# Optimization experiments

Hardware: AMD Instinct MI355X
Metric: run time of the kernel (lower is better)

## Reference

```python
import jax, jax.numpy as jnp
import numpy as np

N_IN, N_OUT = 1024, 4096
D_IN = 1024          # next power of two of N_IN (no padding needed)
STACK = 4            # ceil(N_OUT / D_IN)
BATCH = 8192


def fwht0(x):
    """Unnormalized fast Walsh-Hadamard transform along axis 0 of a (D, C) matrix."""
    D, C = x.shape
    h = 1
    while h < D:
        y = x.reshape(D // (2 * h), 2, h, C)
        a, b = y[:, 0], y[:, 1]
        x = jnp.stack([a + b, a - b], axis=1).reshape(D, C)
        h *= 2
    return x


def sample_block(s1, s2, g_mu, g_rho, eps):
    # W = diag(s1) @ H @ diag(g_tilde) @ H @ diag(s2)
    g_tilde = g_mu + jax.nn.softplus(g_rho) * eps            # (D,)
    Hs2 = fwht0(jnp.diag(s2))                                # H @ diag(s2)
    W = s1[:, None] * fwht0(g_tilde[:, None] * Hs2)          # (D, D)
    return W


def setup_inputs() -> dict:
    key = jax.random.key(0)
    k = jax.random.split(key, 6)
    return {
        "x": jax.random.normal(k[0], (BATCH, N_IN), dtype=jnp.float32),
        "s1": jax.random.normal(k[1], (STACK, D_IN), dtype=jnp.float32),
        "s2": jax.random.normal(k[2], (STACK, D_IN), dtype=jnp.float32),
        "g_mu": jax.random.normal(k[3], (STACK, D_IN), dtype=jnp.float32),
        "g_rho": jax.random.uniform(k[4], (STACK, D_IN), dtype=jnp.float32) - 3.0,
        "eps": jax.random.normal(k[5], (STACK, D_IN), dtype=jnp.float32),
    }


def reference(x, s1, s2, g_mu, g_rho, eps):
    # Sample all stacked square blocks and concatenate rows -> (D_out, D_in)
    Ws = jax.vmap(sample_block)(s1, s2, g_mu, g_rho, eps)    # (stack, D, D)
    W = Ws.reshape(STACK * D_IN, D_IN)                       # (D_out, D_in)
    # Pad input to D_in (no-op here since N_IN == D_IN, kept for fidelity)
    x_padded = jnp.pad(x, ((0, 0), (0, D_IN - N_IN)))
    out = x_padded @ W.T                                     # (B, D_out)
    return out[..., :N_OUT]
```

## Files before the change

kernel.cpp:

```cpp
#include <hip/hip_runtime.h>
#include <math.h>

#define D_IN   1024
#define STACKN 4
#define BATCHN 8192
#define OUTW   (STACKN * D_IN)

__device__ __forceinline__ float softplus_f(float x) {
    return fmaxf(x, 0.0f) + log1pf(expf(-fabsf(x)));
}

__device__ __forceinline__ void fwht1024(float v[16], int lane) {
    #pragma unroll
    for (int m = 1; m <= 8; m <<= 1) {
        #pragma unroll
        for (int r = 0; r < 16; ++r) {
            if (!(r & m)) {
                float a = v[r], b = v[r ^ m];
                v[r]     = a + b;
                v[r ^ m] = a - b;
            }
        }
    }
    #pragma unroll
    for (int m = 1; m <= 32; m <<= 1) {
        const float sgn = (lane & m) ? -1.0f : 1.0f;
        #pragma unroll
        for (int r = 0; r < 16; ++r) {
            float t = __shfl_xor(v[r], m, 64);
            v[r] = fmaf(v[r], sgn, t);
        }
    }
}

__global__ __launch_bounds__(256) void whvi_fwht_kernel(
    const float* __restrict__ x,
    const float* __restrict__ s1,
    const float* __restrict__ s2,
    const float* __restrict__ g_mu,
    const float* __restrict__ g_rho,
    const float* __restrict__ eps,
    float* __restrict__ out)
{
    const int lane = threadIdx.x & 63;
    const int wave = threadIdx.x >> 6;
    const int s    = blockIdx.y;

    float s1v[16], s2v[16], gv[16];
    #pragma unroll
    for (int r = 0; r < 16; ++r) {
        const int i = s * D_IN + ((r >> 2) << 8) + (lane << 2) + (r & 3);
        s1v[r] = s1[i];
        s2v[r] = s2[i];
        gv[r]  = fmaf(softplus_f(g_rho[i]), eps[i], g_mu[i]);
    }

    for (int row = (blockIdx.x << 2) + wave; row < BATCHN; row += (gridDim.x << 2)) {
        const float* __restrict__ xr = x + (size_t)row * D_IN;
        float v[16];

        #pragma unroll
        for (int k = 0; k < 4; ++k) {
            float4 t = *(const float4*)(xr + (k << 8) + (lane << 2));
            v[k*4+0] = t.x * s2v[k*4+0];
            v[k*4+1] = t.y * s2v[k*4+1];
            v[k*4+2] = t.z * s2v[k*4+2];
            v[k*4+3] = t.w * s2v[k*4+3];
        }

        fwht1024(v, lane);

        #pragma unroll
        for (int r = 0; r < 16; ++r) v[r] *= gv[r];

        fwht1024(v, lane);

        float* __restrict__ orow = out + (size_t)row * OUTW + s * D_IN;
        #pragma unroll
        for (int k = 0; k < 4; ++k) {
            float4 t = make_float4(v[k*4+0] * s1v[k*4+0],
                                   v[k*4+1] * s1v[k*4+1],
                                   v[k*4+2] * s1v[k*4+2],
                                   v[k*4+3] * s1v[k*4+3]);
            *(float4*)(orow + (k << 8) + (lane << 2)) = t;
        }
    }
}

extern "C" void kernel_launch(void* const* d_in, const int* in_sizes, int n_in,
                              void* d_out, int out_size, void* d_ws, size_t ws_size,
                              hipStream_t stream) {
    const float* x     = (const float*)d_in[0];
    const float* s1    = (const float*)d_in[1];
    const float* s2    = (const float*)d_in[2];
    const float* g_mu  = (const float*)d_in[3];
    const float* g_rho = (const float*)d_in[4];
    const float* eps   = (const float*)d_in[5];
    float* out = (float*)d_out;

    dim3 grid(512, STACKN);
    whvi_fwht_kernel<<<grid, 256, 0, stream>>>(x, s1, s2, g_mu, g_rho, eps, out);
}
```

Before: 204.3 us.

## Load each x row once for all stacks and use DPP/permlane butterflies

Restructures the grid so each wave processes one batch row across all four stacks, reading x once instead of four times. It replaces the __shfl_xor butterflies in the FWHT with DPP moves, ds_swizzle and permlane16/32 swaps to cut cross-lane exchange cost. The g_tilde softplus is precomputed in a small prep kernel into workspace when workspace is available. In exchange there is an extra kernel launch, the per-stack parameters are reloaded per row, and the grid-stride loop is gone.

```diff
diff --git a/kernel.cpp b/kernel.cpp
--- a/kernel.cpp
+++ b/kernel.cpp
@@ -6,11 +6,20 @@
 #define BATCHN 8192
 #define OUTW   (STACKN * D_IN)
 
-__device__ __forceinline__ float softplus_f(float x) {
-    return fmaxf(x, 0.0f) + log1pf(expf(-fabsf(x)));
+typedef int iv2 __attribute__((ext_vector_type(2)));
+
+__device__ __forceinline__ int   f2i(float x){ union{float f;int i;}u; u.f=x; return u.i; }
+__device__ __forceinline__ float i2f(int x){ union{float f;int i;}u; u.i=x; return u.f; }
+
+template<int CTRL>
+__device__ __forceinline__ float dpp_mov(float v){
+    return i2f(__builtin_amdgcn_update_dpp(0, f2i(v), CTRL, 0xF, 0xF, false));
 }
 
-__device__ __forceinline__ void fwht1024(float v[16], int lane) {
+__device__ __forceinline__ void fwht1024(float v[16],
+                                         float sg1, float sg2,
+                                         float sg4, float sg8)
+{
     #pragma unroll
     for (int m = 1; m <= 8; m <<= 1) {
         #pragma unroll
@@ -22,67 +31,127 @@
             }
         }
     }
+
     #pragma unroll
-    for (int m = 1; m <= 32; m <<= 1) {
-        const float sgn = (lane & m) ? -1.0f : 1.0f;
-        #pragma unroll
-        for (int r = 0; r < 16; ++r) {
-            float t = __shfl_xor(v[r], m, 64);
-            v[r] = fmaf(v[r], sgn, t);
-        }
+    for (int r = 0; r < 16; ++r) {
+        float t = dpp_mov<0xB1>(v[r]);
+        v[r] = fmaf(v[r], sg1, t);
+    }
+    #pragma unroll
+    for (int r = 0; r < 16; ++r) {
+        float t = dpp_mov<0x4E>(v[r]);
+        v[r] = fmaf(v[r], sg2, t);
+    }
+    #pragma unroll
+    for (int r = 0; r < 16; ++r) {
+        float t = i2f(__builtin_amdgcn_ds_swizzle(f2i(v[r]), 0x101F));
+        v[r] = fmaf(v[r], sg4, t);
+    }
+    #pragma unroll
+    for (int r = 0; r < 16; ++r) {
+        float t = dpp_mov<0x128>(v[r]);
+        v[r] = fmaf(v[r], sg8, t);
+    }
+    #pragma unroll
+    for (int r = 0; r < 16; r += 2) {
+        iv2 p = __builtin_amdgcn_permlane16_swap(f2i(v[r]), f2i(v[r+1]), false, false);
+        float a = i2f(p[0]), b = i2f(p[1]);
+        float s = a + b, d = a - b;
+        iv2 q = __builtin_amdgcn_permlane16_swap(f2i(s), f2i(d), false, false);
+        v[r]   = i2f(q[0]);
+        v[r+1] = i2f(q[1]);
+    }
+    #pragma unroll
+    for (int r = 0; r < 16; r += 2) {
+        iv2 p = __builtin_amdgcn_permlane32_swap(f2i(v[r]), f2i(v[r+1]), false, false);
+        float a = i2f(p[0]), b = i2f(p[1]);
+        float s = a + b, d = a - b;
+        iv2 q = __builtin_amdgcn_permlane32_swap(f2i(s), f2i(d), false, false);
+        v[r]   = i2f(q[0]);
+        v[r+1] = i2f(q[1]);
     }
 }
 
-__global__ __launch_bounds__(256) void whvi_fwht_kernel(
+__global__ __launch_bounds__(256) void whvi_prep(
+    const float* __restrict__ g_mu, const float* __restrict__ g_rho,
+    const float* __restrict__ eps, float* __restrict__ gt)
+{
+    const int i = blockIdx.x * 256 + threadIdx.x;
+    const float r  = g_rho[i];
+    const float sp = fmaxf(r, 0.0f) + log1pf(expf(-fabsf(r)));
+    gt[i] = fmaf(sp, eps[i], g_mu[i]);
+}
+
+template<bool USE_WS>
+__global__ __launch_bounds__(256) void whvi_main(
     const float* __restrict__ x,
     const float* __restrict__ s1,
     const float* __restrict__ s2,
     const float* __restrict__ g_mu,
     const float* __restrict__ g_rho,
     const float* __restrict__ eps,
+    const float* __restrict__ gt,
     float* __restrict__ out)
 {
     const int lane = threadIdx.x & 63;
-    const int wave = threadIdx.x >> 6;
-    const int s    = blockIdx.y;
+    const int row  = (blockIdx.x << 2) + (threadIdx.x >> 6);
 
-    float s1v[16], s2v[16], gv[16];
+    const float sg1 = (lane & 1) ? -1.0f : 1.0f;
+    const float sg2 = (lane & 2) ? -1.0f : 1.0f;
+    const float sg4 = (lane & 4) ? -1.0f : 1.0f;
+    const float sg8 = (lane & 8) ? -1.0f : 1.0f;
+
+    const float* __restrict__ xr = x + (size_t)row * D_IN;
+    float xv[16];
     #pragma unroll
-    for (int r = 0; r < 16; ++r) {
-        const int i = s * D_IN + ((r >> 2) << 8) + (lane << 2) + (r & 3);
-        s1v[r] = s1[i];
-        s2v[r] = s2[i];
-        gv[r]  = fmaf(softplus_f(g_rho[i]), eps[i], g_mu[i]);
+    for (int k = 0; k < 4; ++k) {
+        float4 t = *(const float4*)(xr + (k << 8) + (lane << 2));
+        xv[k*4+0] = t.x; xv[k*4+1] = t.y; xv[k*4+2] = t.z; xv[k*4+3] = t.w;
     }
 
-    for (int row = (blockIdx.x << 2) + wave; row < BATCHN; row += (gridDim.x << 2)) {
-        const float* __restrict__ xr = x + (size_t)row * D_IN;
-        float v[16];
+    float* __restrict__ orow = out + (size_t)row * OUTW;
+
+    #pragma unroll
+    for (int s = 0; s < STACKN; ++s) {
+        const int pb = s * D_IN + (lane << 2);
+        float s2v[16], gv[16], s1v[16], v[16];
+        #pragma unroll
+        for (int k = 0; k < 4; ++k) {
+            float4 t2 = *(const float4*)(s2 + pb + (k << 8));
+            s2v[k*4+0] = t2.x; s2v[k*4+1] = t2.y; s2v[k*4+2] = t2.z; s2v[k*4+3] = t2.w;
+            float4 t1 = *(const float4*)(s1 + pb + (k << 8));
+            s1v[k*4+0] = t1.x; s1v[k*4+1] = t1.y; s1v[k*4+2] = t1.z; s1v[k*4+3] = t1.w;
+            if (USE_WS) {
+                float4 tg = *(const float4*)(gt + pb + (k << 8));
+                gv[k*4+0] = tg.x; gv[k*4+1] = tg.y; gv[k*4+2] = tg.z; gv[k*4+3] = tg.w;
+            } else {
+                #pragma unroll
+                for (int c = 0; c < 4; ++c) {
+                    const int i = pb + (k << 8) + c;
+                    const float rr = g_rho[i];
+                    const float sp = fmaxf(rr, 0.0f) + log1pf(expf(-fabsf(rr)));
+                    gv[k*4+c] = fmaf(sp, eps[i], g_mu[i]);
+                }
+            }
+        }
 
         #pragma unroll
-        for (int k = 0; k < 4; ++k) {
-            float4 t = *(const float4*)(xr + (k << 8) + (lane << 2));
-            v[k*4+0] = t.x * s2v[k*4+0];
-            v[k*4+1] = t.y * s2v[k*4+1];
-            v[k*4+2] = t.z * s2v[k*4+2];
-            v[k*4+3] = t.w * s2v[k*4+3];
-        }
+        for (int r = 0; r < 16; ++r) v[r] = xv[r] * s2v[r];
 
-        fwht1024(v, lane);
+        fwht1024(v, sg1, sg2, sg4, sg8);
 
         #pragma unroll
         for (int r = 0; r < 16; ++r) v[r] *= gv[r];
 
-        fwht1024(v, lane);
+        fwht1024(v, sg1, sg2, sg4, sg8);
 
-        float* __restrict__ orow = out + (size_t)row * OUTW + s * D_IN;
         #pragma unroll
         for (int k = 0; k < 4; ++k) {
             float4 t = make_float4(v[k*4+0] * s1v[k*4+0],
                                    v[k*4+1] * s1v[k*4+1],
                                    v[k*4+2] * s1v[k*4+2],
                                    v[k*4+3] * s1v[k*4+3]);
-            *(float4*)(orow + (k << 8) + (lane << 2)) = t;
+            *(float4*)(orow + s * D_IN + (k << 8) + (lane << 2)) = t;
         }
     }
 }
@@ -98,6 +167,12 @@
     const float* eps   = (const float*)d_in[5];
     float* out = (float*)d_out;
 
-    dim3 grid(512, STACKN);
-    whvi_fwht_kernel<<<grid, 256, 0, stream>>>(x, s1, s2, g_mu, g_rho, eps, out);
+    const bool use_ws = ws_size >= (size_t)(STACKN * D_IN * sizeof(float));
+    if (use_ws) {
+        float* gt = (float*)d_ws;
+        whvi_prep<<<STACKN * D_IN / 256, 256, 0, stream>>>(g_mu, g_rho, eps, gt);
+        whvi_main<true><<<BATCHN / 4, 256, 0, stream>>>(x, s1, s2, g_mu, g_rho, eps, gt, out);
+    } else {
+        whvi_main<false><<<BATCHN / 4, 256, 0, stream>>>(x, s1, s2, g_mu, g_rho, eps, nullptr, out);
+    }
 }
```

After: 178.5 us. 1.14x faster.
